# Optimization experiments

Hardware: AMD Instinct MI355X
Metric: run time of the kernel (lower is better)

Reference implementation:

```python
import math
import jax, jax.numpy as jnp
import numpy as np

DIM = 512
STYLE_DIM = 512
WS = 8
RES = 64
HEADS = 16
SHIFT = WS // 2
B = 8
EPS = 1e-5


def _rel_pos_index(ws):
    # Faithful replica of the (non-standard) index construction in the source.
    coords = np.stack(np.meshgrid(np.arange(ws), np.arange(ws), indexing='ij')).reshape(2, -1)
    rc = (coords[:, :, None] - coords[:, None, :]).transpose(1, 2, 0).astype(np.int64)
    rc[:, :, 0] += ws - 1
    rc[:, :, 1] += ws - 1
    rc[:, :, 0] += 2 * ws - 1
    return jnp.asarray(rc.sum(-1))  # (ws*ws, ws*ws)


def _attn_mask2(res, ws):
    shift = ws // 2
    m = np.zeros((res, res), dtype=np.float32)
    cnt = 0
    for hs in [slice(0, -ws), slice(-ws, -shift), slice(-shift, None)]:
        for wsl in [slice(0, -ws), slice(-ws, -shift), slice(-shift, None)]:
            m[hs, wsl] = cnt
            cnt += 1
    mw = m.reshape(res // ws, ws, res // ws, ws).transpose(0, 2, 1, 3).reshape(-1, ws * ws)
    am = mw[:, None, :] - mw[:, :, None]  # (nW, N, N)
    return jnp.asarray(np.where(am != 0, -100.0, 0.0).astype(np.float32))


_RPI = _rel_pos_index(WS)
_MASK2 = _attn_mask2(RES, WS)


def _win_part(x, ws):
    Bc, H, W, C = x.shape
    x = x.reshape(Bc, H // ws, ws, W // ws, ws, C).transpose(0, 1, 3, 2, 4, 5)
    return x.reshape(-1, ws * ws, C)


def _win_rev(x, ws, H, W):
    nH, nW = H // ws, W // ws
    C = x.shape[-1]
    x = x.reshape(-1, nH, nW, ws, ws, C).transpose(0, 1, 3, 2, 4, 5)
    return x.reshape(-1, H, W, C)


def _adain(x, style, w, b):
    # x: (B, N, C); InstanceNorm1d over the token dim N per channel (biased var, no affine).
    scale = 1.0 / math.sqrt(w.shape[1])
    s = style @ (w * scale).T + b  # (B, 2C)
    C = x.shape[-1]
    gamma, beta = s[:, :C], s[:, C:]
    mean = x.mean(axis=1, keepdims=True)
    var = x.var(axis=1, keepdims=True)
    xn = (x - mean) / jnp.sqrt(var + EPS)
    return gamma[:, None, :] * xn + beta[:, None, :]


def _window_attn(q, k, v, ws, heads, rpb, rpi, mask):
    # q/k/v: (B, H, W, C)
    C = q.shape[-1]
    hd = C // heads
    qk_scale = hd ** -0.5
    qw = _win_part(q, ws)  # (Bw, N, C)
    kw = _win_part(k, ws)
    vw = _win_part(v, ws)
    Bw, N, _ = qw.shape
    qw = qw.reshape(Bw, N, heads, hd).transpose(0, 2, 1, 3)
    kw = kw.reshape(Bw, N, heads, hd).transpose(0, 2, 1, 3)
    vw = vw.reshape(Bw, N, heads, hd).transpose(0, 2, 1, 3)
    attn = jnp.einsum('bhnd,bhmd->bhnm', qw, kw) * qk_scale
    bias = rpb[rpi.reshape(-1)].reshape(N, N, heads).transpose(2, 0, 1)  # (h, N, N)
    attn = attn + bias[None]
    if mask is not None:
        nW = mask.shape[0]
        attn = attn.reshape(Bw // nW, nW, heads, N, N) + mask[None, :, None]
        attn = attn.reshape(Bw, heads, N, N)
    attn = jax.nn.softmax(attn, axis=-1)
    out = jnp.einsum('bhnm,bhmd->bhnd', attn, vw)
    return out.transpose(0, 2, 1, 3).reshape(Bw, N, C)


def _forward(x, style, ada1_w, ada1_b, qkv_w, qkv_b, rpb1, rpb2,
             proj_w, proj_b, ada2_w, ada2_b, mlp_w1, mlp_b1, mlp_w2, mlp_b2):
    H = W = RES
    Bc, N, C = x.shape
    shortcut = x
    xn = _adain(x, style, ada1_w, ada1_b)
    qkv = xn @ qkv_w.T + qkv_b  # (B, N, 3C)
    qkv = qkv.reshape(Bc, N, 3, C).transpose(2, 0, 1, 3).reshape(3, Bc, H, W, C)
    qkv1 = qkv[..., : C // 2]
    qkv2 = qkv[..., C // 2:]
    qkv2 = jnp.roll(qkv2, shift=(-SHIFT, -SHIFT), axis=(2, 3))
    x1 = _window_attn(qkv1[0], qkv1[1], qkv1[2], WS, HEADS // 2, rpb1, _RPI, None)
    x2 = _window_attn(qkv2[0], qkv2[1], qkv2[2], WS, HEADS // 2, rpb2, _RPI, _MASK2)
    x1 = _win_rev(x1, WS, H, W)
    x2 = _win_rev(x2, WS, H, W)
    x2 = jnp.roll(x2, shift=(SHIFT, SHIFT), axis=(1, 2))
    out = jnp.concatenate([x1, x2], axis=-1).reshape(Bc, N, C)
    out = out @ proj_w.T + proj_b
    out = shortcut + out
    xn2 = _adain(out, style, ada2_w, ada2_b)
    h = xn2 @ mlp_w1.T + mlp_b1
    h = jax.nn.gelu(h, approximate=False)  # erf-based gelu matches source
    h = h @ mlp_w2.T + mlp_b2
    return out + h


def setup_inputs() -> dict:
    key = jax.random.key(0)
    ks = jax.random.split(key, 16)
    rn = lambda k, shp, s: jax.random.normal(k, shp, dtype=jnp.float32) * s
    return {
        'x': rn(ks[0], (B, RES * RES, DIM), 1.0),
        'style': rn(ks[1], (B, STYLE_DIM), 1.0),
        'ada1_w': rn(ks[2], (2 * DIM, STYLE_DIM), 1.0),
        'ada1_b': rn(ks[3], (2 * DIM,), 0.02),
        'qkv_w': rn(ks[4], (3 * DIM, DIM), 0.02),
        'qkv_b': rn(ks[5], (3 * DIM,), 0.02),
        'rpb1': rn(ks[6], ((2 * WS - 1) ** 2, HEADS // 2), 0.02),
        'rpb2': rn(ks[7], ((2 * WS - 1) ** 2, HEADS // 2), 0.02),
        'proj_w': rn(ks[8], (DIM, DIM), 0.02),
        'proj_b': rn(ks[9], (DIM,), 0.02),
        'ada2_w': rn(ks[10], (2 * DIM, STYLE_DIM), 1.0),
        'ada2_b': rn(ks[11], (2 * DIM,), 0.02),
        'mlp_w1': rn(ks[12], (4 * DIM, DIM), 0.02),
        'mlp_b1': rn(ks[13], (4 * DIM,), 0.02),
        'mlp_w2': rn(ks[14], (DIM, 4 * DIM), 0.02),
        'mlp_b2': rn(ks[15], (DIM,), 0.02),
    }


def reference(x, style, ada1_w, ada1_b, qkv_w, qkv_b, rpb1, rpb2,
              proj_w, proj_b, ada2_w, ada2_b, mlp_w1, mlp_b1, mlp_w2, mlp_b2):
    return _forward(x, style, ada1_w, ada1_b, qkv_w, qkv_b, rpb1, rpb2,
                    proj_w, proj_b, ada2_w, ada2_b, mlp_w1, mlp_b1, mlp_w2, mlp_b2)
```

## Files before the change

### kernel.cpp

```cpp
#include <hip/hip_runtime.h>
#include <math.h>

typedef __attribute__((ext_vector_type(8))) short short8;
typedef __attribute__((ext_vector_type(4))) float f32x4;
typedef unsigned short ushort_t;
typedef unsigned long long ull_t;

__device__ __forceinline__ float bf2f(ushort_t u) {
    return __uint_as_float(((unsigned int)u) << 16);
}
__device__ __forceinline__ ushort_t f2bf(float f) {
    unsigned int u = __float_as_uint(f);
    unsigned int r = u + 0x7fffu + ((u >> 16) & 1u);
    return (ushort_t)(r >> 16);
}
__device__ __forceinline__ unsigned cvt_pk_bf16(float lo, float hi) {
    unsigned r;
    asm volatile("v_cvt_pk_bf16_f32 %0, %1, %2" : "=v"(r) : "v"(lo), "v"(hi));
    return r;
}

__device__ __forceinline__ void async_cp16(const void* g, void* l) {
    __builtin_amdgcn_global_load_lds((const __attribute__((address_space(1))) void*)g,
                                     (__attribute__((address_space(3))) void*)l, 16, 0, 0);
}

__device__ __forceinline__ float fast_gelu(float v) {
    float u2 = 2.0f * v * (0.7978845608028654f + 0.0356774081f * v * v);
    float e = __expf(u2);
    float r = 1.0f / (e + 1.0f);
    return v - v * r;
}

__global__ __launch_bounds__(256) void conv_zero(
        const float* __restrict__ qkv_w, ushort_t* __restrict__ qkv_wb,
        const float* __restrict__ proj_w, ushort_t* __restrict__ proj_wb,
        const float* __restrict__ w1, ushort_t* __restrict__ w1b,
        const float* __restrict__ w2, ushort_t* __restrict__ w2b,
        float* __restrict__ psum2, float* __restrict__ psq2,
        const float* __restrict__ rpb1, const float* __restrict__ rpb2,
        float* __restrict__ tbl0, float* __restrict__ tbl1) {
    int i = blockIdx.x * 256 + threadIdx.x;
    if (i < 786432) {
        qkv_wb[i] = f2bf(qkv_w[i]);
    } else if (i < 1048576) {
        int j = i - 786432; proj_wb[j] = f2bf(proj_w[j]);
    } else if (i < 2097152) {
        int j = i - 1048576; w1b[j] = f2bf(w1[j]);
    } else if (i < 3145728) {
        int j = i - 2097152; w2b[j] = f2bf(w2[j]);
    } else if (i < 3153920) {
        int j = i - 3145728;
        psum2[j] = 0.f; psq2[j] = 0.f;
    } else {
        int t = i - 3153920;
        if (t < 32768) {
            int h = t >> 12, ij = t & 4095;
            int qi = ij >> 6, kj = ij & 63;
            int idx = ((qi >> 3) - (kj >> 3)) + ((qi & 7) - (kj & 7)) + 29;
            tbl0[t] = rpb1[idx * 8 + h];
        } else {
            int u = t - 32768;
            int ij = u & 4095;
            int cls = (u >> 12) & 3;
            int h = u >> 14;
            int qi = ij >> 6, kj = ij & 63;
            int idx = ((qi >> 3) - (kj >> 3)) + ((qi & 7) - (kj & 7)) + 29;
            float v = rpb2[idx * 8 + h];
            int gh_i = (cls & 2) ? (((qi >> 3) < 4) ? 1 : 2) : 0;
            int gw_i = (cls & 1) ? (((qi & 7) < 4) ? 1 : 2) : 0;
            int gh_j = (cls & 2) ? (((kj >> 3) < 4) ? 1 : 2) : 0;
            int gw_j = (cls & 1) ? (((kj & 7) < 4) ? 1 : 2) : 0;
            if (gh_i * 3 + gw_i != gh_j * 3 + gw_j) v -= 100.f;
            tbl1[u] = v;
        }
    }
}

__global__ __launch_bounds__(256) void style_kernel(const float* __restrict__ style,
        const float* __restrict__ w1, const float* __restrict__ b1,
        const float* __restrict__ w2, const float* __restrict__ b2,
        float* __restrict__ s1, float* __restrict__ s2) {
    int t = blockIdx.x * 256 + threadIdx.x;
    int which = t >> 13;
    int idx = t & 8191;
    int b = idx >> 10, j = idx & 1023;
    const float* w = which ? w2 : w1;
    const float* bb = which ? b2 : b1;
    const float* st = style + b * 512;
    const float* wr = w + (size_t)j * 512;
    float acc = 0.f;
    for (int k = 0; k < 512; ++k) acc += st[k] * wr[k];
    float v = acc * 0.04419417382415922f + bb[j];
    (which ? s2 : s1)[idx] = v;
}

__global__ __launch_bounds__(512) void stats_part(const float* __restrict__ x,
        float* __restrict__ psum, float* __restrict__ psq) {
    int b = blockIdx.x >> 5;
    int ch = blockIdx.x & 31;
    int c = threadIdx.x;
    const float* p = x + ((size_t)b * 4096 + (size_t)ch * 128) * 512 + c;
    float s = 0.f, q = 0.f;
    for (int t = 0; t < 128; ++t) {
        float v = p[(size_t)t * 512];
        s += v; q += v * v;
    }
    psum[(size_t)blockIdx.x * 512 + c] = s;
    psq [(size_t)blockIdx.x * 512 + c] = q;
}

__global__ __launch_bounds__(256) void stats_fin(const float* __restrict__ psum,
        const float* __restrict__ psq, float* __restrict__ mean, float* __restrict__ rstd) {
    int i = blockIdx.x * 256 + threadIdx.x;
    int b = i >> 9, c = i & 511;
    float s = 0.f, q = 0.f;
    for (int ch = 0; ch < 32; ++ch) {
        s += psum[(size_t)(b * 32 + ch) * 512 + c];
        q += psq [(size_t)(b * 32 + ch) * 512 + c];
    }
    float m = s * (1.f / 4096.f);
    float v = q * (1.f / 4096.f) - m * m;
    mean[i] = m;
    rstd[i] = rsqrtf(v + 1e-5f);
}

__global__ __launch_bounds__(256) void stats_fin2(const float* __restrict__ psum2,
        const float* __restrict__ psq2, float* __restrict__ mean, float* __restrict__ rstd) {
    int i = blockIdx.x * 256 + threadIdx.x;
    float m = psum2[i] * (1.f / 4096.f);
    float v = psq2[i] * (1.f / 4096.f) - m * m;
    mean[i] = m;
    rstd[i] = rsqrtf(v + 1e-5f);
}

__global__ __launch_bounds__(256) void adain_kernel(const float* __restrict__ x,
        const float* __restrict__ s, const float* __restrict__ mean,
        const float* __restrict__ rstd, ushort_t* __restrict__ xn) {
    size_t i4 = (size_t)blockIdx.x * 256 + threadIdx.x;
    size_t e = i4 * 4;
    int b = (int)(e >> 21);
    int c = (int)(e & 511);
    float4 xv = *(const float4*)(x + e);
    float vals[4] = {xv.x, xv.y, xv.z, xv.w};
    ushort_t o[4];
#pragma unroll
    for (int j = 0; j < 4; ++j) {
        int cc = c + j;
        float g  = s[b * 1024 + cc];
        float be = s[b * 1024 + 512 + cc];
        float mn = mean[b * 512 + cc];
        float rs = rstd[b * 512 + cc];
        o[j] = f2bf(g * (vals[j] - mn) * rs + be);
    }
    ull_t packed = (ull_t)o[0] |
        ((ull_t)o[1] << 16) | ((ull_t)o[2] << 32) | ((ull_t)o[3] << 48);
    *(ull_t*)(xn + e) = packed;
}

template<int EPI>
__global__ __launch_bounds__(512, 2) void gemm256(
        const ushort_t* __restrict__ A, const ushort_t* __restrict__ Bw,
        const float* __restrict__ bias, const float* __restrict__ resid,
        float* __restrict__ outf, ushort_t* __restrict__ outh,
        float* __restrict__ psum2, float* __restrict__ psq2,
        int N, int K, int gridN, int ntiles, int lnt) {
    __shared__ ushort_t lds[65536];
    const int tid  = threadIdx.x;
    const int lane = tid & 63;
    const int wave = tid >> 6;
    const int wm = wave >> 2, wn = wave & 3;
    const int lm = lane & 15;
    const int kg = lane >> 4;
    const int nt = 1 << lnt;
    const int tpb = ntiles >> 8;

    const int orig = blockIdx.x;
    const int wgid = (orig & 7) * 32 + (orig >> 3);

    unsigned int lo0 = lm * 128 + ((kg * 16) ^ ((lm & 7) << 4));
    unsigned int lo1 = lo0 ^ 64;
    unsigned int vA0 = wm * 16384 + lo0;
    unsigned int vA1 = wm * 16384 + lo1;
    unsigned int vB0 = 65536 + (wn >> 1) * 16384 + (wn & 1) * 8192 + lo0;
    unsigned int vB1 = 65536 + (wn >> 1) * 16384 + (wn & 1) * 8192 + lo1;
    const char* ldsc = (const char*)lds;

    int off[2][2];
#pragma unroll
    for (int rnd = 0; rnd < 2; ++rnd) {
        int chunk = tid + rnd * 512;
        int row = chunk >> 3;
        int g = chunk & 7;
        int gsw = g ^ (row & 7);
#pragma unroll
        for (int h = 0; h < 2; ++h)
            off[h][rnd] = (h * 128 + row) * K + gsw * 8;
    }

    f32x4 acc[8][4];
#pragma unroll
    for (int m = 0; m < 8; ++m)
#pragma unroll
        for (int n = 0; n < 4; ++n)
#pragma unroll
            for (int r = 0; r < 4; ++r) acc[m][n][r] = 0.f;

    auto stage = [&](const ushort_t* __restrict__ mat, long bcur, long bnxt,
                     int dslot, int h, int tt, int isB) {
        long mb = (tt < nt) ? bcur : bnxt;
        int kt = tt & (nt - 1);
        const ushort_t* base = mat + mb + (kt << 6);
        ushort_t* dst = (ushort_t*)lds + isB * 32768 + dslot * 16384 + h * 8192 + tid * 8;
#pragma unroll
        for (int rnd = 0; rnd < 2; ++rnd)
            async_cp16(base + off[h][rnd], dst + rnd * 4096);
    };

    int tcur = wgid;
    int bm = tcur / gridN, bn = tcur - bm * gridN;
    long Am = (long)bm * 256 * K;
    long Bn = (long)bn * 256 * K;

    stage(A,  Am, Am, 0, 0, 0, 0); stage(A,  Am, Am, 0, 1, 0, 0);
    stage(Bw, Bn, Bn, 0, 0, 0, 1); stage(Bw, Bn, Bn, 0, 1, 0, 1);
    stage(Bw, Bn, Bn, 1, 0, 1, 1); stage(Bw, Bn, Bn, 1, 1, 1, 1);
    asm volatile("s_waitcnt vmcnt(4)" ::: "memory");
    __builtin_amdgcn_sched_barrier(0);
    __builtin_amdgcn_s_barrier();
    asm volatile("" ::: "memory");

    for (int ti = 0; ti < tpb; ++ti) {
        int tnxt = (ti + 1 < tpb) ? tcur + 256 : tcur;
        int bm2 = tnxt / gridN, bn2 = tnxt - bm2 * gridN;
        long Am2 = (long)bm2 * 256 * K;
        long Bn2 = (long)bn2 * 256 * K;

#pragma unroll 2
        for (int t = 0; t < nt; ++t) {
            const int c = t & 1;
            short8 bfr[4][2];
#pragma unroll
            for (int q = 0; q < 4; ++q) {
                short8 af[2][2];
#pragma unroll
                for (int mq = 0; mq < 2; ++mq) {
                    af[mq][0] = *(const short8*)(ldsc + vA0 + (q * 4096 + mq * 2048));
                    af[mq][1] = *(const short8*)(ldsc + vA1 + (q * 4096 + mq * 2048));
                }
                if (q == 0) {
#pragma unroll
                    for (int n = 0; n < 4; ++n) {
                        bfr[n][0] = *(const short8*)(ldsc + vB0 + n * 2048);
                        bfr[n][1] = *(const short8*)(ldsc + vB1 + n * 2048);
                    }
                }
                if      (q == 0) stage(A,  Am, Am2, c ^ 1, 0, t + 1, 0);
                else if (q == 1) stage(A,  Am, Am2, c ^ 1, 1, t + 1, 0);
                else if (q == 2) stage(Bw, Bn, Bn2, c,     0, t + 2, 1);
                else             stage(Bw, Bn, Bn2, c,     1, t + 2, 1);

                __builtin_amdgcn_s_setprio(1);
#pragma unroll
                for (int mq = 0; mq < 2; ++mq)
#pragma unroll
                    for (int n = 0; n < 4; ++n)
#pragma unroll
                        for (int ks = 0; ks < 2; ++ks)
                            acc[q * 2 + mq][n] = __builtin_amdgcn_mfma_f32_16x16x32_bf16(
                                af[mq][ks], bfr[n][ks], acc[q * 2 + mq][n], 0, 0, 0);
                __builtin_amdgcn_s_setprio(0);
                if (q == 3) {
                    asm volatile("s_waitcnt vmcnt(4)" ::: "memory");
                    __builtin_amdgcn_sched_barrier(0);
                }
                __builtin_amdgcn_s_barrier();
                asm volatile("" ::: "memory");
            }
            vA0 ^= 32768u; vA1 ^= 32768u; vB0 ^= 32768u; vB1 ^= 32768u;
        }

        const long tile_m = (long)bm * 256;
        const long tile_n = (long)bn * 256;
        float csum[4], csq[4];
        if (EPI == 1) {
#pragma unroll
            for (int n = 0; n < 4; ++n) { csum[n] = 0.f; csq[n] = 0.f; }
        }
#pragma unroll
        for (int m = 0; m < 8; ++m) {
            long row0 = tile_m + wm * 128 + m * 16 + kg * 4;
#pragma unroll
            for (int n = 0; n < 4; ++n) {
                long col = tile_n + wn * 64 + n * 16 + lm;
                float bb = bias[col];
#pragma unroll
                for (int r = 0; r < 4; ++r) {
                    long o = (row0 + r) * (long)N + col;
                    float v = acc[m][n][r] + bb;
                    if (EPI == 0) {
                        outh[o] = f2bf(v);
                    } else if (EPI == 1) {
                        float w = v + resid[o];
                        outf[o] = w;
                        csum[n] += w; csq[n] += w * w;
                    } else if (EPI == 2) {
                        outh[o] = f2bf(fast_gelu(v));
                    } else {
                        outf[o] += v;
                    }
                    acc[m][n][r] = 0.f;
                }
            }
        }
        if (EPI == 1) {
            int b = (int)(tile_m >> 12);
#pragma unroll
            for (int n = 0; n < 4; ++n) {
                int col = (int)(tile_n + wn * 64 + n * 16 + lm);
                atomicAdd(&psum2[b * 512 + col], csum[n]);
                atomicAdd(&psq2 [b * 512 + col], csq[n]);
            }
        }

        tcur = tnxt; bm = bm2; bn = bn2; Am = Am2; Bn = Bn2;
    }
}

__global__ __launch_bounds__(256) void attn_mfma(const ushort_t* __restrict__ qkv,
        const float* __restrict__ tbl0, const float* __restrict__ tbl1,
        ushort_t* __restrict__ attno) {
    __shared__ ushort_t lds[27648];
    const int tid = threadIdx.x;
    const int lane = tid & 63;
    const int wave = tid >> 6;
    const int job = blockIdx.x * 4 + wave;
    const int branch = job >> 12;
    const int w_idx  = (job >> 3) & 511;
    const int head   = job & 7;
    const int b = w_idx >> 6, win = w_idx & 63;
    const int wh = win >> 3, ww = win & 7;
    const int c0 = branch * 256 + head * 32;
    const int i_lo = lane & 15;
    const int kg = lane >> 4;

    ushort_t* Vt = lds + wave * 6912;
    ushort_t* P  = lds + wave * 6912 + 2304;

    auto tokof = [&](int p) {
        int hh = wh * 8 + (p >> 3), wp = ww * 8 + (p & 7);
        if (branch) { hh = (hh + 4) & 63; wp = (wp + 4) & 63; }
        return b * 4096 + hh * 64 + wp;
    };

    {
        const ushort_t* vp = qkv + (size_t)tokof(lane) * 1536 + 1024 + c0;
        short8 v0 = *(const short8*)(vp);
        short8 v1 = *(const short8*)(vp + 8);
        short8 v2 = *(const short8*)(vp + 16);
        short8 v3 = *(const short8*)(vp + 24);
#pragma unroll
        for (int e = 0; e < 8; ++e) {
            Vt[(e     ) * 72 + lane] = (ushort_t)v0[e];
            Vt[(e +  8) * 72 + lane] = (ushort_t)v1[e];
            Vt[(e + 16) * 72 + lane] = (ushort_t)v2[e];
            Vt[(e + 24) * 72 + lane] = (ushort_t)v3[e];
        }
    }

    short8 kf[4], qf[4];
#pragma unroll
    for (int m = 0; m < 4; ++m) {
        size_t rowb = (size_t)tokof(m * 16 + i_lo) * 1536;
        kf[m] = *(const short8*)(qkv + rowb + 512 + c0 + kg * 8);
        qf[m] = *(const short8*)(qkv + rowb + c0 + kg * 8);
    }

    f32x4 s[4][4];
#pragma unroll
    for (int mj = 0; mj < 4; ++mj)
#pragma unroll
        for (int ni = 0; ni < 4; ++ni)
#pragma unroll
            for (int r = 0; r < 4; ++r) s[mj][ni][r] = 0.f;
#pragma unroll
    for (int mj = 0; mj < 4; ++mj)
#pragma unroll
        for (int ni = 0; ni < 4; ++ni)
            s[mj][ni] = __builtin_amdgcn_mfma_f32_16x16x32_bf16(kf[mj], qf[ni], s[mj][ni], 0, 0, 0);

    const float* tb;
    if (branch == 0) {
        tb = tbl0 + head * 4096;
    } else {
        int cls = ((wh == 7) ? 2 : 0) | ((ww == 7) ? 1 : 0);
        tb = tbl1 + (head * 4 + cls) * 4096;
    }
#pragma unroll
    for (int ni = 0; ni < 4; ++ni) {
        int i = ni * 16 + i_lo;
#pragma unroll
        for (int mj = 0; mj < 4; ++mj) {
            float4 bv = *(const float4*)(tb + i * 64 + mj * 16 + kg * 4);
            s[mj][ni][0] = s[mj][ni][0] * 0.17677669529663687f + bv.x;
            s[mj][ni][1] = s[mj][ni][1] * 0.17677669529663687f + bv.y;
            s[mj][ni][2] = s[mj][ni][2] * 0.17677669529663687f + bv.z;
            s[mj][ni][3] = s[mj][ni][3] * 0.17677669529663687f + bv.w;
        }
    }

    float mx[4], rs[4];
#pragma unroll
    for (int ni = 0; ni < 4; ++ni) {
        float m = -1e30f;
#pragma unroll
        for (int mj = 0; mj < 4; ++mj)
#pragma unroll
            for (int r = 0; r < 4; ++r) m = fmaxf(m, s[mj][ni][r]);
        m = fmaxf(m, __shfl_xor(m, 16));
        m = fmaxf(m, __shfl_xor(m, 32));
        mx[ni] = m;
    }
#pragma unroll
    for (int ni = 0; ni < 4; ++ni) {
        float sum = 0.f;
#pragma unroll
        for (int mj = 0; mj < 4; ++mj)
#pragma unroll
            for (int r = 0; r < 4; ++r) {
                float e = __expf(s[mj][ni][r] - mx[ni]);
                s[mj][ni][r] = e;
                sum += e;
            }
        sum += __shfl_xor(sum, 16);
        sum += __shfl_xor(sum, 32);
        rs[ni] = sum;
    }

#pragma unroll
    for (int ni = 0; ni < 4; ++ni) {
        int i = ni * 16 + i_lo;
#pragma unroll
        for (int mj = 0; mj < 4; ++mj) {
            unsigned w0 = cvt_pk_bf16(s[mj][ni][0], s[mj][ni][1]);
            unsigned w1 = cvt_pk_bf16(s[mj][ni][2], s[mj][ni][3]);
            ull_t w = (ull_t)w0 | ((ull_t)w1 << 32);
            *(ull_t*)&P[i * 72 + mj * 16 + kg * 4] = w;
        }
    }
    asm volatile("s_waitcnt lgkmcnt(0)" ::: "memory");
    __builtin_amdgcn_sched_barrier(0);

    short8 va[2][2];
    short8 pb[4][2];
#pragma unroll
    for (int md = 0; md < 2; ++md)
#pragma unroll
        for (int ks = 0; ks < 2; ++ks)
            va[md][ks] = *(const short8*)&Vt[(md * 16 + i_lo) * 72 + ks * 32 + kg * 8];
#pragma unroll
    for (int ni = 0; ni < 4; ++ni)
#pragma unroll
        for (int ks = 0; ks < 2; ++ks)
            pb[ni][ks] = *(const short8*)&P[(ni * 16 + i_lo) * 72 + ks * 32 + kg * 8];

    f32x4 o[2][4];
#pragma unroll
    for (int md = 0; md < 2; ++md)
#pragma unroll
        for (int ni = 0; ni < 4; ++ni)
#pragma unroll
            for (int r = 0; r < 4; ++r) o[md][ni][r] = 0.f;
#pragma unroll
    for (int md = 0; md < 2; ++md)
#pragma unroll
        for (int ni = 0; ni < 4; ++ni)
#pragma unroll
            for (int ks = 0; ks < 2; ++ks)
                o[md][ni] = __builtin_amdgcn_mfma_f32_16x16x32_bf16(va[md][ks], pb[ni][ks], o[md][ni], 0, 0, 0);

#pragma unroll
    for (int ni = 0; ni < 4; ++ni) {
        float inv = 1.f / rs[ni];
        ushort_t* op = attno + (size_t)tokof(ni * 16 + i_lo) * 512 + c0;
#pragma unroll
        for (int md = 0; md < 2; ++md) {
            ushort_t h0 = f2bf(o[md][ni][0] * inv);
            ushort_t h1 = f2bf(o[md][ni][1] * inv);
            ushort_t h2 = f2bf(o[md][ni][2] * inv);
            ushort_t h3 = f2bf(o[md][ni][3] * inv);
            ull_t w = (ull_t)h0 | ((ull_t)h1 << 16) | ((ull_t)h2 << 32) | ((ull_t)h3 << 48);
            *(ull_t*)(op + md * 16 + kg * 4) = w;
        }
    }
}

extern "C" void kernel_launch(void* const* d_in, const int* in_sizes, int n_in,
                              void* d_out, int out_size, void* d_ws, size_t ws_size,
                              hipStream_t stream) {
    const float* x      = (const float*)d_in[0];
    const float* style  = (const float*)d_in[1];
    const float* ada1_w = (const float*)d_in[2];
    const float* ada1_b = (const float*)d_in[3];
    const float* qkv_w  = (const float*)d_in[4];
    const float* qkv_b  = (const float*)d_in[5];
    const float* rpb1   = (const float*)d_in[6];
    const float* rpb2   = (const float*)d_in[7];
    const float* proj_w = (const float*)d_in[8];
    const float* proj_b = (const float*)d_in[9];
    const float* ada2_w = (const float*)d_in[10];
    const float* ada2_b = (const float*)d_in[11];
    const float* mlp_w1 = (const float*)d_in[12];
    const float* mlp_b1 = (const float*)d_in[13];
    const float* mlp_w2 = (const float*)d_in[14];
    const float* mlp_b2 = (const float*)d_in[15];
    float* outf = (float*)d_out;

    char* W = (char*)d_ws;
    ushort_t* qkvb    = (ushort_t*)(W);
    ushort_t* attno   = (ushort_t*)(W + 100663296);
    ushort_t* hbuf    = (ushort_t*)(W);
    ushort_t* xn      = (ushort_t*)(W + 134217728);
    ushort_t* qkv_wb  = (ushort_t*)(W + 167772160);
    ushort_t* proj_wb = (ushort_t*)(W + 167772160 + 1572864);
    ushort_t* w1b     = (ushort_t*)(W + 167772160 + 2097152);
    ushort_t* w2b     = (ushort_t*)(W + 167772160 + 4194304);
    float* freg  = (float*)(W + 167772160 + 6291456);
    float* s1    = freg;
    float* s2    = freg + 8192;
    float* mean1 = freg + 16384;
    float* rstd1 = freg + 20480;
    float* mean2 = freg + 24576;
    float* rstd2 = freg + 28672;
    float* psum  = freg + 32768;
    float* psq   = freg + 163840;
    float* psum2 = freg + 294912;
    float* psq2  = freg + 303104;
    float* tbl0  = freg + 311296;
    float* tbl1  = freg + 344064;

    conv_zero<<<12960, 256, 0, stream>>>(qkv_w, qkv_wb, proj_w, proj_wb,
                                         mlp_w1, w1b, mlp_w2, w2b, psum2, psq2,
                                         rpb1, rpb2, tbl0, tbl1);

    style_kernel<<<64, 256, 0, stream>>>(style, ada1_w, ada1_b, ada2_w, ada2_b, s1, s2);

    stats_part<<<256, 512, 0, stream>>>(x, psum, psq);
    stats_fin<<<16, 256, 0, stream>>>(psum, psq, mean1, rstd1);
    adain_kernel<<<16384, 256, 0, stream>>>(x, s1, mean1, rstd1, xn);

    gemm256<0><<<256, 512, 0, stream>>>(xn, qkv_wb, qkv_b, nullptr, nullptr, qkvb,
                                        nullptr, nullptr, 1536, 512, 6, 768, 3);

    attn_mfma<<<2048, 256, 0, stream>>>(qkvb, tbl0, tbl1, attno);

    gemm256<1><<<256, 512, 0, stream>>>(attno, proj_wb, proj_b, x, outf, nullptr,
                                        psum2, psq2, 512, 512, 2, 256, 3);

    stats_fin2<<<16, 256, 0, stream>>>(psum2, psq2, mean2, rstd2);
    adain_kernel<<<16384, 256, 0, stream>>>(outf, s2, mean2, rstd2, xn);

    gemm256<2><<<256, 512, 0, stream>>>(xn, w1b, mlp_b1, nullptr, nullptr, hbuf,
                                        nullptr, nullptr, 2048, 512, 8, 1024, 3);
    gemm256<3><<<256, 512, 0, stream>>>(hbuf, w2b, mlp_b2, nullptr, outf, nullptr,
                                        nullptr, nullptr, 512, 2048, 2, 256, 5);
}
```

Measured before the change: 423.1 us.

## Replace 256x256 GEMM tiles with 128x128 tiles and simpler double buffering

```diff
diff --git a/kernel.cpp b/kernel.cpp
--- a/kernel.cpp
+++ b/kernel.cpp
@@ -159,17 +159,17 @@
 }
 
 template<int EPI>
-__global__ __launch_bounds__(512, 2) void gemm256(
+__global__ __launch_bounds__(256, 3) void gemm128(
         const ushort_t* __restrict__ A, const ushort_t* __restrict__ Bw,
         const float* __restrict__ bias, const float* __restrict__ resid,
         float* __restrict__ outf, ushort_t* __restrict__ outh,
         float* __restrict__ psum2, float* __restrict__ psq2,
         int N, int K, int gridN, int ntiles, int lnt) {
-    __shared__ ushort_t lds[65536];
+    __shared__ ushort_t lds[16384];
     const int tid  = threadIdx.x;
     const int lane = tid & 63;
     const int wave = tid >> 6;
-    const int wm = wave >> 2, wn = wave & 3;
+    const int wm = wave >> 1, wn = wave & 1;
     const int lm = lane & 15;
     const int kg = lane >> 4;
     const int nt = 1 << lnt;
@@ -178,54 +178,46 @@
     const int orig = blockIdx.x;
     const int wgid = (orig & 7) * 32 + (orig >> 3);
 
-    unsigned int lo0 = lm * 128 + ((kg * 16) ^ ((lm & 7) << 4));
-    unsigned int lo1 = lo0 ^ 64;
-    unsigned int vA0 = wm * 16384 + lo0;
-    unsigned int vA1 = wm * 16384 + lo1;
-    unsigned int vB0 = 65536 + (wn >> 1) * 16384 + (wn & 1) * 8192 + lo0;
-    unsigned int vB1 = 65536 + (wn >> 1) * 16384 + (wn & 1) * 8192 + lo1;
+    const unsigned int swz = ((lm >> 1) & 3) << 4;
+    unsigned int vA = (wm * 64 + lm) * 64 + ((kg * 16) ^ swz);
+    unsigned int vB = 16384 + (wn * 64 + lm) * 64 + ((kg * 16) ^ swz);
     const char* ldsc = (const char*)lds;
 
-    int off[2][2];
+    int off[2];
 #pragma unroll
     for (int rnd = 0; rnd < 2; ++rnd) {
-        int chunk = tid + rnd * 512;
-        int row = chunk >> 3;
-        int g = chunk & 7;
-        int gsw = g ^ (row & 7);
-#pragma unroll
-        for (int h = 0; h < 2; ++h)
-            off[h][rnd] = (h * 128 + row) * K + gsw * 8;
-    }
-
-    f32x4 acc[8][4];
-#pragma unroll
-    for (int m = 0; m < 8; ++m)
+        int chunk = tid + rnd * 256;
+        int row = chunk >> 2;
+        int gslot = (chunk & 3) ^ ((row >> 1) & 3);
+        off[rnd] = row * K + gslot * 8;
+    }
+
+    f32x4 acc[4][4];
+#pragma unroll
+    for (int m = 0; m < 4; ++m)
 #pragma unroll
         for (int n = 0; n < 4; ++n)
 #pragma unroll
             for (int r = 0; r < 4; ++r) acc[m][n][r] = 0.f;
 
     auto stage = [&](const ushort_t* __restrict__ mat, long bcur, long bnxt,
-                     int dslot, int h, int tt, int isB) {
+                     int dslot, int tt, int isB) {
         long mb = (tt < nt) ? bcur : bnxt;
         int kt = tt & (nt - 1);
-        const ushort_t* base = mat + mb + (kt << 6);
-        ushort_t* dst = (ushort_t*)lds + isB * 32768 + dslot * 16384 + h * 8192 + tid * 8;
-#pragma unroll
-        for (int rnd = 0; rnd < 2; ++rnd)
-            async_cp16(base + off[h][rnd], dst + rnd * 4096);
+        const ushort_t* base = mat + mb + (kt << 5);
+        ushort_t* dst = (ushort_t*)lds + isB * 8192 + dslot * 4096 + tid * 8;
+        async_cp16(base + off[0], dst);
+        async_cp16(base + off[1], dst + 2048);
     };
 
     int tcur = wgid;
     int bm = tcur / gridN, bn = tcur - bm * gridN;
-    long Am = (long)bm * 256 * K;
-    long Bn = (long)bn * 256 * K;
-
-    stage(A,  Am, Am, 0, 0, 0, 0); stage(A,  Am, Am, 0, 1, 0, 0);
-    stage(Bw, Bn, Bn, 0, 0, 0, 1); stage(Bw, Bn, Bn, 0, 1, 0, 1);
-    stage(Bw, Bn, Bn, 1, 0, 1, 1); stage(Bw, Bn, Bn, 1, 1, 1, 1);
-    asm volatile("s_waitcnt vmcnt(4)" ::: "memory");
+    long Am = (long)bm * 128 * K;
+    long Bn = (long)bn * 128 * K;
+
+    stage(A,  Am, Am, 0, 0, 0);
+    stage(Bw, Bn, Bn, 0, 0, 1);
+    asm volatile("s_waitcnt vmcnt(0)" ::: "memory");
     __builtin_amdgcn_sched_barrier(0);
     __builtin_amdgcn_s_barrier();
     asm volatile("" ::: "memory");
@@ -233,63 +225,49 @@
     for (int ti = 0; ti < tpb; ++ti) {
         int tnxt = (ti + 1 < tpb) ? tcur + 256 : tcur;
         int bm2 = tnxt / gridN, bn2 = tnxt - bm2 * gridN;
-        long Am2 = (long)bm2 * 256 * K;
-        long Bn2 = (long)bn2 * 256 * K;
+        long Am2 = (long)bm2 * 128 * K;
+        long Bn2 = (long)bn2 * 128 * K;
 
 #pragma unroll 2
         for (int t = 0; t < nt; ++t) {
             const int c = t & 1;
-            short8 bfr[4][2];
-#pragma unroll
-            for (int q = 0; q < 4; ++q) {
-                short8 af[2][2];
-#pragma unroll
-                for (int mq = 0; mq < 2; ++mq) {
-                    af[mq][0] = *(const short8*)(ldsc + vA0 + (q * 4096 + mq * 2048));
-                    af[mq][1] = *(const short8*)(ldsc + vA1 + (q * 4096 + mq * 2048));
-                }
-                if (q == 0) {
-#pragma unroll
-                    for (int n = 0; n < 4; ++n) {
-                        bfr[n][0] = *(const short8*)(ldsc + vB0 + n * 2048);
-                        bfr[n][1] = *(const short8*)(ldsc + vB1 + n * 2048);
-                    }
-                }
-                if      (q == 0) stage(A,  Am, Am2, c ^ 1, 0, t + 1, 0);
-                else if (q == 1) stage(A,  Am, Am2, c ^ 1, 1, t + 1, 0);
-                else if (q == 2) stage(Bw, Bn, Bn2, c,     0, t + 2, 1);
-                else             stage(Bw, Bn, Bn2, c,     1, t + 2, 1);
-
-                __builtin_amdgcn_s_setprio(1);
-#pragma unroll
-                for (int mq = 0; mq < 2; ++mq)
-#pragma unroll
-                    for (int n = 0; n < 4; ++n)
-#pragma unroll
-                        for (int ks = 0; ks < 2; ++ks)
-                            acc[q * 2 + mq][n] = __builtin_amdgcn_mfma_f32_16x16x32_bf16(
-                                af[mq][ks], bfr[n][ks], acc[q * 2 + mq][n], 0, 0, 0);
-                __builtin_amdgcn_s_setprio(0);
-                if (q == 3) {
-                    asm volatile("s_waitcnt vmcnt(4)" ::: "memory");
-                    __builtin_amdgcn_sched_barrier(0);
-                }
-                __builtin_amdgcn_s_barrier();
-                asm volatile("" ::: "memory");
-            }
-            vA0 ^= 32768u; vA1 ^= 32768u; vB0 ^= 32768u; vB1 ^= 32768u;
-        }
-
-        const long tile_m = (long)bm * 256;
-        const long tile_n = (long)bn * 256;
+            stage(A,  Am, Am2, c ^ 1, t + 1, 0);
+            stage(Bw, Bn, Bn2, c ^ 1, t + 1, 1);
+
+            short8 af[4], bfr[4];
+#pragma unroll
+            for (int m = 0; m < 4; ++m)
+                af[m] = *(const short8*)(ldsc + vA + m * 1024);
+#pragma unroll
+            for (int n = 0; n < 4; ++n)
+                bfr[n] = *(const short8*)(ldsc + vB + n * 1024);
+
+            __builtin_amdgcn_s_setprio(1);
+#pragma unroll
+            for (int m = 0; m < 4; ++m)
+#pragma unroll
+                for (int n = 0; n < 4; ++n)
+                    acc[m][n] = __builtin_amdgcn_mfma_f32_16x16x32_bf16(
+                        af[m], bfr[n], acc[m][n], 0, 0, 0);
+            __builtin_amdgcn_s_setprio(0);
+
+            asm volatile("s_waitcnt vmcnt(0)" ::: "memory");
+            __builtin_amdgcn_sched_barrier(0);
+            __builtin_amdgcn_s_barrier();
+            asm volatile("" ::: "memory");
+            vA ^= 8192u; vB ^= 8192u;
+        }
+
+        const long tile_m = (long)bm * 128;
+        const long tile_n = (long)bn * 128;
         float csum[4], csq[4];
         if (EPI == 1) {
 #pragma unroll
             for (int n = 0; n < 4; ++n) { csum[n] = 0.f; csq[n] = 0.f; }
         }
 #pragma unroll
-        for (int m = 0; m < 8; ++m) {
-            long row0 = tile_m + wm * 128 + m * 16 + kg * 4;
+        for (int m = 0; m < 4; ++m) {
+            long row0 = tile_m + wm * 64 + m * 16 + kg * 4;
 #pragma unroll
             for (int n = 0; n < 4; ++n) {
                 long col = tile_n + wn * 64 + n * 16 + lm;
@@ -549,19 +527,19 @@
     stats_fin<<<16, 256, 0, stream>>>(psum, psq, mean1, rstd1);
     adain_kernel<<<16384, 256, 0, stream>>>(x, s1, mean1, rstd1, xn);
 
-    gemm256<0><<<256, 512, 0, stream>>>(xn, qkv_wb, qkv_b, nullptr, nullptr, qkvb,
-                                        nullptr, nullptr, 1536, 512, 6, 768, 3);
+    gemm128<0><<<256, 256, 0, stream>>>(xn, qkv_wb, qkv_b, nullptr, nullptr, qkvb,
+                                        nullptr, nullptr, 1536, 512, 12, 3072, 4);
 
     attn_mfma<<<2048, 256, 0, stream>>>(qkvb, tbl0, tbl1, attno);
 
-    gemm256<1><<<256, 512, 0, stream>>>(attno, proj_wb, proj_b, x, outf, nullptr,
-                                        psum2, psq2, 512, 512, 2, 256, 3);
+    gemm128<1><<<256, 256, 0, stream>>>(attno, proj_wb, proj_b, x, outf, nullptr,
+                                        psum2, psq2, 512, 512, 4, 1024, 4);
 
     stats_fin2<<<16, 256, 0, stream>>>(psum2, psq2, mean2, rstd2);
     adain_kernel<<<16384, 256, 0, stream>>>(outf, s2, mean2, rstd2, xn);
 
-    gemm256<2><<<256, 512, 0, stream>>>(xn, w1b, mlp_b1, nullptr, nullptr, hbuf,
-                                        nullptr, nullptr, 2048, 512, 8, 1024, 3);
-    gemm256<3><<<256, 512, 0, stream>>>(hbuf, w2b, mlp_b2, nullptr, outf, nullptr,
-                                        nullptr, nullptr, 512, 2048, 2, 256, 5);
-}
+    gemm128<2><<<256, 256, 0, stream>>>(xn, w1b, mlp_b1, nullptr, nullptr, hbuf,
+                                        nullptr, nullptr, 2048, 512, 16, 4096, 4);
+    gemm128<3><<<256, 256, 0, stream>>>(hbuf, w2b, mlp_b2, nullptr, outf, nullptr,
+                                        nullptr, nullptr, 512, 2048, 4, 1024, 6);
+}
```

Result: slower. 746.6 us (+76.5%).
